# Performance work log

Hardware: AMD Instinct MI355X
Metric: run time of the kernel (lower is better)

Reference implementation:

```python
import jax, jax.numpy as jnp
import numpy as np

N_ATOMS = 10000
N_PAIRS = 100000
H = 64          # hidden_channels
R = 32          # number_of_radial_basis_functions
MAX_Z = 100
CUTOFF = 0.5    # nm (radial_max_distance), min = 0.0


def cosine_cutoff(d):
    # 0.5*(cos(pi*d/rc)+1) for d < rc else 0
    return jnp.where(d < CUTOFF, 0.5 * (jnp.cos(jnp.pi * d / CUTOFF) + 1.0), 0.0)


def expnormal_rbf(d):
    # ExpNormal smearing (TorchMD/TensorNet style), cutoff_lower = 0
    start = float(np.exp(-CUTOFF))
    means = jnp.linspace(start, 1.0, R, dtype=d.dtype)            # [R]
    beta = (2.0 / R * (1.0 - start)) ** -2
    alpha = 5.0 / CUTOFF
    return jnp.exp(-beta * (jnp.exp(-alpha * d)[:, None] - means) ** 2)  # [P,R]


def vector_to_skewtensor(v):
    x, y, z = v[:, 0], v[:, 1], v[:, 2]
    o = jnp.zeros_like(x)
    return jnp.stack([o, -z, y, z, o, -x, -y, x, o], axis=-1).reshape(-1, 3, 3)


def vector_to_symtensor(v):
    t = v[:, :, None] * v[:, None, :]                              # [P,3,3]
    tr3 = (t[:, 0, 0] + t[:, 1, 1] + t[:, 2, 2]) / 3.0
    return t - tr3[:, None, None] * jnp.eye(3, dtype=v.dtype)


def setup_inputs() -> dict:
    key = jax.random.key(0)
    ks = jax.random.split(key, 20)
    atomic_numbers = jax.random.randint(ks[0], (N_ATOMS,), 0, MAX_Z)
    pair_indices = jax.random.randint(ks[1], (2, N_PAIRS), 0, N_ATOMS)
    r_ij = jax.random.normal(ks[2], (N_PAIRS, 3), dtype=jnp.float32) * 0.12  # ~0.2 nm norms
    d_ij = jnp.linalg.norm(r_ij, axis=-1, keepdims=True) + 1e-6
    s = 0.1
    p = {
        'emb':    jax.random.normal(ks[3], (MAX_Z, H)) * s,
        'emb2_w': jax.random.normal(ks[4], (H, 2 * H)) * s,
        'emb2_b': jnp.zeros((H,)),
        'dp1_w':  jax.random.normal(ks[5], (H, R)) * s,
        'dp1_b':  jnp.zeros((H,)),
        'dp2_w':  jax.random.normal(ks[6], (H, R)) * s,
        'dp2_b':  jnp.zeros((H,)),
        'dp3_w':  jax.random.normal(ks[7], (H, R)) * s,
        'dp3_b':  jnp.zeros((H,)),
        'lt0_w':  jax.random.normal(ks[8], (H, H)) * s,
        'lt1_w':  jax.random.normal(ks[9], (H, H)) * s,
        'lt2_w':  jax.random.normal(ks[10], (H, H)) * s,
        'ls1_w':  jax.random.normal(ks[11], (2 * H, H)) * s,
        'ls1_b':  jnp.zeros((2 * H,)),
        'ls2_w':  jax.random.normal(ks[12], (3 * H, 2 * H)) * s,
        'ls2_b':  jnp.zeros((3 * H,)),
        'ln_g':   jnp.ones((H,)),
        'ln_b':   jnp.zeros((H,)),
    }
    return dict(atomic_numbers=atomic_numbers, pair_indices=pair_indices,
                d_ij=d_ij, r_ij=r_ij, **p)


def reference(atomic_numbers, pair_indices, d_ij, r_ij,
              emb, emb2_w, emb2_b, dp1_w, dp1_b, dp2_w, dp2_b, dp3_w, dp3_b,
              lt0_w, lt1_w, lt2_w, ls1_w, ls1_b, ls2_w, ls2_b, ln_g, ln_b):
    n_atoms = atomic_numbers.shape[0]
    src = pair_indices[0]
    # atomic number message Zij: concat(emb[i], emb[j]) -> Linear
    zi = emb[atomic_numbers]                                      # [N,H]
    zij = jnp.concatenate([zi[src], zi[pair_indices[1]]], axis=-1)  # [P,2H]
    Zij = zij @ emb2_w.T + emb2_b                                 # [P,H]
    d = d_ij[:, 0]                                                # [P]
    unit = r_ij / d_ij                                            # [P,3]
    rc = cosine_cutoff(d)                                         # [P]
    rbf = expnormal_rbf(d) * rc[:, None]                          # [P,R]
    C = rc[:, None] * Zij                                         # [P,H]
    f1 = (rbf @ dp1_w.T + dp1_b) * C                              # [P,H]
    f2 = (rbf @ dp2_w.T + dp2_b) * C * 10.0                       # Angstrom scale
    f3 = (rbf @ dp3_w.T + dp3_b) * C * 100.0
    eye = jnp.eye(3, dtype=r_ij.dtype)
    skew = vector_to_skewtensor(unit)                             # [P,3,3]
    sym = vector_to_symtensor(unit)                               # [P,3,3]
    Iij = f1[:, :, None, None] * eye                              # [P,H,3,3]
    Aij = f2[:, :, None, None] * skew[:, None]
    Sij = f3[:, :, None, None] * sym[:, None]
    I = jax.ops.segment_sum(Iij, src, num_segments=n_atoms)       # [N,H,3,3]
    A = jax.ops.segment_sum(Aij, src, num_segments=n_atoms)
    S = jax.ops.segment_sum(Sij, src, num_segments=n_atoms)
    # tensor_norm -> LayerNorm -> scalar MLP
    tn = jnp.sum((I + A + S) ** 2, axis=(-2, -1))                 # [N,H]
    mu = tn.mean(-1, keepdims=True)
    var = tn.var(-1, keepdims=True)
    norm = (tn - mu) / jnp.sqrt(var + 1e-5) * ln_g + ln_b
    norm = jax.nn.silu(norm @ ls1_w.T + ls1_b)
    norm = jax.nn.silu(norm @ ls2_w.T + ls2_b)                    # [N,3H]
    norm = norm.reshape(-1, H, 3)
    I = jnp.einsum('nhij,gh->ngij', I, lt0_w) * norm[:, :, 0][:, :, None, None]
    A = jnp.einsum('nhij,gh->ngij', A, lt1_w) * norm[:, :, 1][:, :, None, None]
    S = jnp.einsum('nhij,gh->ngij', S, lt2_w) * norm[:, :, 2][:, :, None, None]
    return I + A + S
```

## Files before the change

### kernel.cpp

```cpp
#include <hip/hip_runtime.h>
#include <hip/hip_bf16.h>

#define N_ATOMS 10000
#define N_PAIRS 100000
#define HH 64
#define MAXZ 100

typedef _Float16 h2_t __attribute__((ext_vector_type(2)));

constexpr float RBF_START = 0.6065306597126334f;
constexpr float RBF_STEP  = (1.0f - RBF_START) / 31.0f;
constexpr float RBF_BETA  = 1.0f / ((0.0625f * (1.0f - RBF_START)) * (0.0625f * (1.0f - RBF_START)));
constexpr float LOG2E     = 1.4426950408889634f;
constexpr float NEG_ALPHA_L2 = -10.0f * LOG2E;
constexpr float NEG_BETA_L2  = -RBF_BETA * LOG2E;

#define OFF_EMB   0
#define OFF_W2    6400
#define OFF_B2    14592
#define OFF_D1W   14656
#define OFF_D1B   16704
#define OFF_D2W   16768
#define OFF_D2B   18816
#define OFF_D3W   18880
#define OFF_D3B   20928
#define OFF_LT0   20992
#define OFF_LT1   25088
#define OFF_LT2   29184
#define OFF_L1W   33280
#define OFF_L1B   41472
#define OFF_L2W   41600
#define OFF_L2B   66176
#define OFF_LNG   66368
#define OFF_LNB   66432
#define N_PARAMF  66496

#define PH_DP   0
#define PH_L1   3072
#define PH_L2   7168
#define PH_LT   19456
#define PH_N    25600

#define WS_WF     0
#define WS_CNT    266240
#define WS_OFF    307200
#define WS_CUR    348160
#define WS_T1     389120
#define WS_T2     414720
#define WS_PH     440320
#define WS_DPK    542720
#define WS_ZNL    2142720
#define WS_ACCH   2542720

__device__ __forceinline__ float bf2f(unsigned short u) {
    return __uint_as_float(((unsigned int)u) << 16);
}
__device__ __forceinline__ float fexp2(float x) { return __builtin_amdgcn_exp2f(x); }
__device__ __forceinline__ float fcos2pi(float x) { return __builtin_amdgcn_cosf(x); }
__device__ __forceinline__ float fsilu(float x) { return x / (1.0f + fexp2(-LOG2E * x)); }
__device__ __forceinline__ h2_t u2h(unsigned u) { return __builtin_bit_cast(h2_t, u); }
__device__ __forceinline__ unsigned packh2(float a, float b) {
    h2_t v; v.x = (_Float16)a; v.y = (_Float16)b;
    return __builtin_bit_cast(unsigned, v);
}

#if __has_builtin(__builtin_amdgcn_fdot2)
__device__ __forceinline__ float FDOT2(h2_t a, h2_t b, float c) {
    return __builtin_amdgcn_fdot2(a, b, c, false);
}
#else
__device__ __forceinline__ float FDOT2(h2_t a, h2_t b, float c) {
    return c + (float)a.x * (float)b.x + (float)a.y * (float)b.y;
}
#endif
__device__ __forceinline__ float dot16h(const uint4* w, const uint4* x, float acc) {
    uint4 a = *w, b = *x;
    acc = FDOT2(u2h(a.x), u2h(b.x), acc);
    acc = FDOT2(u2h(a.y), u2h(b.y), acc);
    acc = FDOT2(u2h(a.z), u2h(b.z), acc);
    acc = FDOT2(u2h(a.w), u2h(b.w), acc);
    return acc;
}

__device__ int classify64(const unsigned short* b, int lane) {
    unsigned short x = b[lane];
    int e = (x >> 7) & 0xFF;
    bool implaus = (x != 0) && (e < 96 || e > 133);
    bool zeroeven = ((lane & 1) == 0) && (x == 0);
    unsigned long long mi = __ballot(implaus);
    unsigned long long mz = __ballot(zeroeven);
    if (__popcll(mz) == 32) return 0;
    if (__popcll(mi) >= 8) return 0;
    return 1;
}

__device__ __forceinline__ float ldp(const void* p, int off, int fl) {
    if (fl == 1) return bf2f(((const unsigned short*)p)[off]);
    return ((const float*)p)[off];
}

struct ConvArgs { const void* src[18]; float* dst; };

__global__ void k_prep(ConvArgs a, const int* __restrict__ pidx, int* __restrict__ cnt,
                       float* __restrict__ T1, float* __restrict__ T2,
                       unsigned* __restrict__ PH) {
    const int sizes[18] = {6400,8192,64,2048,64,2048,64,2048,64,4096,4096,4096,8192,128,24576,192,64,64};
    __shared__ int fl;
    if (threadIdx.x < 64) {
        int f = classify64((const unsigned short*)a.src[0], threadIdx.x);
        if (threadIdx.x == 0) fl = f;
    }
    __syncthreads();

    if (blockIdx.x < 391) {
        int t = blockIdx.x * 256 + threadIdx.x;
        if (t < N_PARAMF) {
            int acc = 0, seg = 0, off = t;
            #pragma unroll
            for (int i = 0; i < 18; ++i) {
                if (t >= acc && t < acc + sizes[i]) { seg = i; off = t - acc; }
                acc += sizes[i];
            }
            a.dst[t] = ldp(a.src[seg], off, fl);
        }
        if (t < N_PAIRS) atomicAdd(&cnt[pidx[t]], 1);
        return;
    }

    int zb = blockIdx.x - 391;
    int h = threadIdx.x;
    if (h < 64) {
        float s1 = 0.f, s2 = 0.f;
        #pragma unroll
        for (int k = 0; k < 64; ++k) {
            float e = ldp(a.src[0], zb * HH + k, fl);
            s1 += ldp(a.src[1], h * 128 + k, fl) * e;
            s2 += ldp(a.src[1], h * 128 + 64 + k, fl) * e;
        }
        T1[zb * HH + h] = s1;
        T2[zb * HH + h] = s2;
    }
    int q = zb * 256 + threadIdx.x;
    const void* sp; int off;
    if (q < PH_L1) {
        int w = q >> 10, r = q & 1023;
        sp = a.src[3 + 2 * w];
        off = r * 2;
    } else if (q < PH_L2) {
        sp = a.src[12]; off = (q - PH_L1) * 2;
    } else if (q < PH_LT) {
        sp = a.src[14]; off = (q - PH_L2) * 2;
    } else {
        int tt = q - PH_LT;
        sp = a.src[9 + (tt >> 11)]; off = (tt & 2047) * 2;
    }
    PH[q] = packh2(ldp(sp, off, fl), ldp(sp, off + 1, fl));
}

__global__ void k_scan(const int* __restrict__ cnt, int* __restrict__ offs, int* __restrict__ cur) {
    __shared__ int wsum[16];
    int tid = threadIdx.x;
    int lane = tid & 63, wid = tid >> 6;
    int base = tid * 10;
    int c[10]; int s = 0;
    #pragma unroll
    for (int i = 0; i < 10; ++i) {
        int idx = base + i;
        int v = (idx < N_ATOMS) ? cnt[idx] : 0;
        c[i] = v; s += v;
    }
    int inc = s;
    #pragma unroll
    for (int o = 1; o < 64; o <<= 1) {
        int v = __shfl_up(inc, o);
        if (lane >= o) inc += v;
    }
    if (lane == 63) wsum[wid] = inc;
    __syncthreads();
    int wbase = 0;
    #pragma unroll
    for (int w = 0; w < 16; ++w) {
        int v = wsum[w];
        if (w < wid) wbase += v;
    }
    int run = wbase + (inc - s);
    #pragma unroll
    for (int i = 0; i < 10; ++i) {
        int idx = base + i;
        if (idx < N_ATOMS) { offs[idx] = run; cur[idx] = run; run += c[i]; }
    }
    if (tid == 0) offs[N_ATOMS] = N_PAIRS;
}

__global__ void k_fill(const int* __restrict__ pidx, const int* __restrict__ an,
                       const void* __restrict__ dij_v, const void* __restrict__ rij_v,
                       int* __restrict__ cur,
                       float4* __restrict__ dpack, int* __restrict__ znl) {
    __shared__ int fdr[2];
    if (threadIdx.x < 64) {
        int fd = classify64((const unsigned short*)dij_v, threadIdx.x);
        int fr = classify64((const unsigned short*)rij_v, threadIdx.x);
        if (threadIdx.x == 0) { fdr[0] = fd; fdr[1] = fr; }
    }
    __syncthreads();
    int p = blockIdx.x * 256 + threadIdx.x;
    if (p >= N_PAIRS) return;
    int s = pidx[p];
    int dst = pidx[N_PAIRS + p];
    int pos = atomicAdd(&cur[s], 1);
    float d, rx, ry, rz;
    if (fdr[0] == 1) d = bf2f(((const unsigned short*)dij_v)[p]);
    else             d = ((const float*)dij_v)[p];
    if (fdr[1] == 1) {
        const unsigned short* r = (const unsigned short*)rij_v;
        rx = bf2f(r[3*p]); ry = bf2f(r[3*p+1]); rz = bf2f(r[3*p+2]);
    } else {
        const float* r = (const float*)rij_v;
        rx = r[3*p]; ry = r[3*p+1]; rz = r[3*p+2];
    }
    dpack[pos] = make_float4(rx, ry, rz, d);
    znl[pos] = an[dst];
}

__global__ __launch_bounds__(256, 2) void k_pair(
    const int* __restrict__ an,
    const float* __restrict__ WF,
    const int* __restrict__ offs,
    const float4* __restrict__ dpack, const int* __restrict__ znl,
    const float* __restrict__ T1, const float* __restrict__ T2,
    const unsigned* __restrict__ PH,
    unsigned* __restrict__ accH)
{
    const int wave = threadIdx.x >> 6;
    const int h    = threadIdx.x & 63;
    const int n    = blockIdx.x * 4 + wave;

    unsigned w1u[16], w2u[16], w3u[16];
    {
        const uint4* g1 = (const uint4*)(PH + PH_DP + 0 * 1024 + h * 16);
        const uint4* g2 = (const uint4*)(PH + PH_DP + 1 * 1024 + h * 16);
        const uint4* g3 = (const uint4*)(PH + PH_DP + 2 * 1024 + h * 16);
        #pragma unroll
        for (int k = 0; k < 4; ++k) {
            uint4 a = g1[k]; w1u[4*k] = a.x; w1u[4*k+1] = a.y; w1u[4*k+2] = a.z; w1u[4*k+3] = a.w;
            uint4 b = g2[k]; w2u[4*k] = b.x; w2u[4*k+1] = b.y; w2u[4*k+2] = b.z; w2u[4*k+3] = b.w;
            uint4 c = g3[k]; w3u[4*k] = c.x; w3u[4*k+1] = c.y; w3u[4*k+2] = c.z; w3u[4*k+3] = c.w;
        }
    }
    #pragma unroll
    for (int q = 0; q < 16; ++q)
        asm volatile("" : "+v"(w1u[q]), "+v"(w2u[q]), "+v"(w3u[q]));

    const float ed1 = (WF + OFF_D1B)[h];
    const float ed2 = (WF + OFF_D2B)[h];
    const float ed3 = (WF + OFF_D3B)[h];
    const float zA  = (WF + OFF_B2)[h] + T1[an[n] * HH + h];

    float Is=0.f, sx=0.f, sy=0.f, sz=0.f;
    float Sxx=0.f, Syy=0.f, Szz=0.f, Sxy=0.f, Sxz=0.f, Syz=0.f;

    const int pbeg = offs[n], pend = offs[n + 1];

    const float meanj = RBF_START + RBF_STEP * (float)(h & 31);

    float4 dp_cur = make_float4(0.f, 0.f, 0.f, 1.f);
    float4 dp_nxt = make_float4(0.f, 0.f, 0.f, 1.f);
    float  t2cur  = 0.f;
    int    zn_n   = 0;
    if (pbeg < pend) {
        dp_cur = dpack[pbeg];
        t2cur  = T2[znl[pbeg] * HH + h];
        if (pbeg + 1 < pend) {
            dp_nxt = dpack[pbeg + 1];
            zn_n   = znl[pbeg + 1];
        }
    }

    for (int ii = pbeg; ii < pend; ++ii) {
        const float4 dpv = dp_cur;
        const float  t2v = t2cur;
        dp_cur = dp_nxt;
        if (ii + 2 < pend) dp_nxt = dpack[ii + 2];
        if (ii + 1 < pend) t2cur  = T2[zn_n * HH + h];
        if (ii + 2 < pend) zn_n   = znl[ii + 2];

        float d = dpv.w;
        float inv = 1.0f / d;
        float ux = dpv.x*inv, uy = dpv.y*inv, uz = dpv.z*inv;
        float rc = (d < 0.5f) ? 0.5f * (fcos2pi(d) + 1.0f) : 0.0f;

        float en = fexp2(NEG_ALPHA_L2 * d);
        float t  = en - meanj;
        float r  = fexp2(NEG_BETA_L2 * t * t) * rc;
        float rdn = __shfl_down(r, 1);
        unsigned ru = packh2(r, rdn);
        unsigned rbs[16];
        #pragma unroll
        for (int q = 0; q < 16; ++q)
            rbs[q] = (unsigned)__builtin_amdgcn_readlane((int)ru, 2 * q);

        float g1a = ed1, g2a = ed2, g3a = ed3;
        #pragma unroll
        for (int q = 0; q < 16; ++q) {
            h2_t rb = u2h(rbs[q]);
            g1a = FDOT2(u2h(w1u[q]), rb, g1a);
            g2a = FDOT2(u2h(w2u[q]), rb, g2a);
            g3a = FDOT2(u2h(w3u[q]), rb, g3a);
        }

        float zc = zA + t2v;
        float Cc = rc * zc;
        float f1 = g1a * Cc;
        float f2 = g2a * Cc * 10.0f;
        float f3 = g3a * Cc * 100.0f;

        Is += f1;
        sx += f2 * ux;  sy += f2 * uy;  sz += f2 * uz;
        float qq = (ux*ux + uy*uy + uz*uz) * (1.0f / 3.0f);
        Sxx += f3 * (ux*ux - qq);
        Syy += f3 * (uy*uy - qq);
        Szz += f3 * (uz*uz - qq);
        Sxy += f3 * (ux*uy);
        Sxz += f3 * (ux*uz);
        Syz += f3 * (uy*uz);
    }

    float tn = 3.0f*Is*Is + 2.0f*(sx*sx + sy*sy + sz*sz)
             + Sxx*Sxx + Syy*Syy + Szz*Szz
             + 2.0f*(Sxy*Sxy + Sxz*Sxz + Syz*Syz);
    float s1 = tn, s2 = tn * tn;
    #pragma unroll
    for (int o = 32; o > 0; o >>= 1) {
        s1 += __shfl_xor(s1, o);
        s2 += __shfl_xor(s2, o);
    }
    float mu  = s1 * (1.0f / 64.0f);
    float var = s2 * (1.0f / 64.0f) - mu * mu;
    float nv  = (tn - mu) * rsqrtf(var + 1e-5f) * (WF + OFF_LNG)[h] + (WF + OFF_LNB)[h];

    float vals[11] = {Is, sx, sy, sz, Sxx, Syy, Szz, Sxy, Sxz, Syz, nv};
    #pragma unroll
    for (int c = 0; c < 11; ++c) {
        float pv = __shfl_xor(vals[c], 1);
        if ((h & 1) == 0)
            accH[((n * 11 + c) << 5) + (h >> 1)] = packh2(vals[c], pv);
    }
}

__global__ __launch_bounds__(256, 2) void k_post(
    const float* __restrict__ WF,
    const unsigned* __restrict__ PH,
    const unsigned* __restrict__ accH,
    float* __restrict__ out)
{
    __shared__ __align__(16) unsigned wL2[192 * 68];
    __shared__ __align__(16) unsigned acch[4][12 * 32];
    __shared__ __align__(16) unsigned y1h[4][64];
    __shared__ __align__(16) unsigned y2h[4][96];

    for (int q = threadIdx.x; q < 12288; q += 256) {
        int m = q >> 6, u = q & 63;
        wL2[m * 68 + u] = PH[PH_L2 + q];
    }
    __syncthreads();

    const int wave = threadIdx.x >> 6;
    const int h    = threadIdx.x & 63;
    const int gw   = blockIdx.x * 4 + wave;
    const int GW   = gridDim.x * 4;

    const uint4* l1base = (const uint4*)(PH + PH_L1);
    const uint4* lt0 = (const uint4*)(PH + PH_LT) + h * 8;
    const uint4* lt1 = (const uint4*)(PH + PH_LT + 2048) + h * 8;
    const uint4* lt2 = (const uint4*)(PH + PH_LT + 4096) + h * 8;

    for (int n = gw; n < N_ATOMS; n += GW) {
        if (h < 32) {
            #pragma unroll
            for (int c = 0; c < 11; ++c)
                acch[wave][c * 32 + h] = accH[((n * 11 + c) << 5) + h];
        }
        __builtin_amdgcn_wave_barrier();

        const uint4* nvh = (const uint4*)&acch[wave][10 * 32];

        float ya = (WF + OFF_L1B)[h];
        float yb = (WF + OFF_L1B)[h + 64];
        {
            const uint4* ra = l1base + h * 8;
            const uint4* rb = l1base + (h + 64) * 8;
            #pragma unroll
            for (int k = 0; k < 8; ++k) {
                ya = dot16h(ra + k, nvh + k, ya);
                yb = dot16h(rb + k, nvh + k, yb);
            }
        }
        ya = fsilu(ya); yb = fsilu(yb);
        {
            float pa = __shfl_xor(ya, 1);
            float pb = __shfl_xor(yb, 1);
            if ((h & 1) == 0) {
                y1h[wave][(h >> 1)]      = packh2(ya, pa);
                y1h[wave][32 + (h >> 1)] = packh2(yb, pb);
            }
        }
        __builtin_amdgcn_wave_barrier();

        const uint4* y1p = (const uint4*)&y1h[wave][0];
        float z0 = (WF + OFF_L2B)[h];
        float z1 = (WF + OFF_L2B)[h + 64];
        float z2 = (WF + OFF_L2B)[h + 128];
        {
            const uint4* r0 = (const uint4*)&wL2[(h)       * 68];
            const uint4* r1 = (const uint4*)&wL2[(h + 64)  * 68];
            const uint4* r2 = (const uint4*)&wL2[(h + 128) * 68];
            #pragma unroll
            for (int k = 0; k < 16; ++k) {
                uint4 x = y1p[k];
                uint4 a0 = r0[k], a1 = r1[k], a2 = r2[k];
                z0 = FDOT2(u2h(a0.x), u2h(x.x), z0); z0 = FDOT2(u2h(a0.y), u2h(x.y), z0);
                z0 = FDOT2(u2h(a0.z), u2h(x.z), z0); z0 = FDOT2(u2h(a0.w), u2h(x.w), z0);
                z1 = FDOT2(u2h(a1.x), u2h(x.x), z1); z1 = FDOT2(u2h(a1.y), u2h(x.y), z1);
                z1 = FDOT2(u2h(a1.z), u2h(x.z), z1); z1 = FDOT2(u2h(a1.w), u2h(x.w), z1);
                z2 = FDOT2(u2h(a2.x), u2h(x.x), z2); z2 = FDOT2(u2h(a2.y), u2h(x.y), z2);
                z2 = FDOT2(u2h(a2.z), u2h(x.z), z2); z2 = FDOT2(u2h(a2.w), u2h(x.w), z2);
            }
        }
        z0 = fsilu(z0); z1 = fsilu(z1); z2 = fsilu(z2);
        {
            float p0 = __shfl_xor(z0, 1);
            float p1 = __shfl_xor(z1, 1);
            float p2 = __shfl_xor(z2, 1);
            if ((h & 1) == 0) {
                y2h[wave][(h >> 1)]      = packh2(z0, p0);
                y2h[wave][32 + (h >> 1)] = packh2(z1, p1);
                y2h[wave][64 + (h >> 1)] = packh2(z2, p2);
            }
        }
        __builtin_amdgcn_wave_barrier();

        float n0, n1, n2;
        {
            int i0 = 3 * h;
            unsigned u0 = y2h[wave][i0 >> 1];
            unsigned u1 = y2h[wave][(i0 >> 1) + 1];
            h2_t a = u2h(u0), b = u2h(u1);
            if (i0 & 1) { n0 = (float)a.y; n1 = (float)b.x; n2 = (float)b.y; }
            else        { n0 = (float)a.x; n1 = (float)a.y; n2 = (float)b.x; }
        }

        const uint4* aI  = (const uint4*)&acch[wave][0];
        const uint4* aAx = (const uint4*)&acch[wave][32];
        const uint4* aAy = (const uint4*)&acch[wave][64];
        const uint4* aAz = (const uint4*)&acch[wave][96];
        const uint4* aXX = (const uint4*)&acch[wave][128];
        const uint4* aYY = (const uint4*)&acch[wave][160];
        const uint4* aZZ = (const uint4*)&acch[wave][192];
        const uint4* aXY = (const uint4*)&acch[wave][224];
        const uint4* aXZ = (const uint4*)&acch[wave][256];
        const uint4* aYZ = (const uint4*)&acch[wave][288];

        float P0=0.f, PAx=0.f, PAy=0.f, PAz=0.f;
        float Q0=0.f, Q1=0.f, Q2=0.f, Q3=0.f, Q4=0.f, Q5=0.f;
        #pragma unroll
        for (int k = 0; k < 8; ++k) {
            P0  = dot16h(lt0 + k, aI  + k, P0);
            PAx = dot16h(lt1 + k, aAx + k, PAx);
            PAy = dot16h(lt1 + k, aAy + k, PAy);
            PAz = dot16h(lt1 + k, aAz + k, PAz);
            Q0  = dot16h(lt2 + k, aXX + k, Q0);
            Q1  = dot16h(lt2 + k, aYY + k, Q1);
            Q2  = dot16h(lt2 + k, aZZ + k, Q2);
            Q3  = dot16h(lt2 + k, aXY + k, Q3);
            Q4  = dot16h(lt2 + k, aXZ + k, Q4);
            Q5  = dot16h(lt2 + k, aYZ + k, Q5);
        }
        float Iv = P0 * n0;
        float Ax = PAx * n1, Ay = PAy * n1, Az = PAz * n1;
        float Xx = Q0 * n2, Yy = Q1 * n2, Zz = Q2 * n2;
        float Xy = Q3 * n2, Xz = Q4 * n2, Yz = Q5 * n2;

        float* o = out + (size_t)n * 576 + h * 9;
        o[0] =  Iv + Xx;  o[1] = -Az + Xy;  o[2] =  Ay + Xz;
        o[3] =  Az + Xy;  o[4] =  Iv + Yy;  o[5] = -Ax + Yz;
        o[6] = -Ay + Xz;  o[7] =  Ax + Yz;  o[8] =  Iv + Zz;
        __builtin_amdgcn_wave_barrier();
    }
}

extern "C" void kernel_launch(void* const* d_in, const int* in_sizes, int n_in,
                              void* d_out, int out_size, void* d_ws, size_t ws_size,
                              hipStream_t stream) {
    const int* an   = (const int*)d_in[0];
    const int* pidx = (const int*)d_in[1];

    char* ws = (char*)d_ws;
    float*    WF    = (float*)(ws + WS_WF);
    int*      cnt   = (int*)(ws + WS_CNT);
    int*      offs  = (int*)(ws + WS_OFF);
    int*      cur   = (int*)(ws + WS_CUR);
    float*    T1    = (float*)(ws + WS_T1);
    float*    T2    = (float*)(ws + WS_T2);
    unsigned* PH    = (unsigned*)(ws + WS_PH);
    float4*   dpack = (float4*)(ws + WS_DPK);
    int*      znl   = (int*)(ws + WS_ZNL);
    unsigned* accH  = (unsigned*)(ws + WS_ACCH);
    float*    out   = (float*)d_out;

    hipMemsetAsync(cnt, 0, N_ATOMS * sizeof(int), stream);

    ConvArgs ca;
    for (int i = 0; i < 18; ++i) ca.src[i] = d_in[4 + i];
    ca.dst = WF;
    k_prep<<<491, 256, 0, stream>>>(ca, pidx, cnt, T1, T2, PH);
    k_scan<<<1, 1024, 0, stream>>>(cnt, offs, cur);
    k_fill<<<(N_PAIRS + 255) / 256, 256, 0, stream>>>(pidx, an, d_in[2], d_in[3],
                                                      cur, dpack, znl);
    k_pair<<<2500, 256, 0, stream>>>(an, WF, offs, dpack, znl, T1, T2, PH, accH);
    k_post<<<256, 256, 0, stream>>>(WF, PH, accH, out);
}
```

Baseline: 235.8 us.

## Replace global-atomic counting sort with per-block LDS histograms and prefix offsets

```diff
diff --git a/kernel.cpp b/kernel.cpp
--- a/kernel.cpp
+++ b/kernel.cpp
@@ -5,6 +5,9 @@
 #define N_PAIRS 100000
 #define HH 64
 #define MAXZ 100
+
+#define NB_HIST 64
+#define PPB 1563
 
 typedef _Float16 h2_t __attribute__((ext_vector_type(2)));
 
@@ -44,13 +47,14 @@
 #define WS_WF     0
 #define WS_CNT    266240
 #define WS_OFF    307200
-#define WS_CUR    348160
 #define WS_T1     389120
 #define WS_T2     414720
 #define WS_PH     440320
 #define WS_DPK    542720
 #define WS_ZNL    2142720
 #define WS_ACCH   2542720
+#define WS_H      WS_ACCH
+#define WS_SUB    (WS_ACCH + 2560000)
 
 __device__ __forceinline__ float bf2f(unsigned short u) {
     return __uint_as_float(((unsigned int)u) << 16);
@@ -101,10 +105,11 @@
 
 struct ConvArgs { const void* src[18]; float* dst; };
 
-__global__ void k_prep(ConvArgs a, const int* __restrict__ pidx, int* __restrict__ cnt,
+__global__ void k_prep(ConvArgs a, const int* __restrict__ pidx,
                        float* __restrict__ T1, float* __restrict__ T2,
-                       unsigned* __restrict__ PH) {
+                       unsigned* __restrict__ PH, int* __restrict__ H) {
     const int sizes[18] = {6400,8192,64,2048,64,2048,64,2048,64,4096,4096,4096,8192,128,24576,192,64,64};
+    __shared__ int lh[N_ATOMS];
     __shared__ int fl;
     if (threadIdx.x < 64) {
         int f = classify64((const unsigned short*)a.src[0], threadIdx.x);
@@ -112,7 +117,7 @@
     }
     __syncthreads();
 
-    if (blockIdx.x < 391) {
+    if (blockIdx.x < 260) {
         int t = blockIdx.x * 256 + threadIdx.x;
         if (t < N_PARAMF) {
             int acc = 0, seg = 0, off = t;
@@ -123,41 +128,67 @@
             }
             a.dst[t] = ldp(a.src[seg], off, fl);
         }
-        if (t < N_PAIRS) atomicAdd(&cnt[pidx[t]], 1);
         return;
     }
 
-    int zb = blockIdx.x - 391;
-    int h = threadIdx.x;
-    if (h < 64) {
-        float s1 = 0.f, s2 = 0.f;
-        #pragma unroll
-        for (int k = 0; k < 64; ++k) {
-            float e = ldp(a.src[0], zb * HH + k, fl);
-            s1 += ldp(a.src[1], h * 128 + k, fl) * e;
-            s2 += ldp(a.src[1], h * 128 + 64 + k, fl) * e;
-        }
-        T1[zb * HH + h] = s1;
-        T2[zb * HH + h] = s2;
-    }
-    int q = zb * 256 + threadIdx.x;
-    const void* sp; int off;
-    if (q < PH_L1) {
-        int w = q >> 10, r = q & 1023;
-        sp = a.src[3 + 2 * w];
-        off = r * 2;
-    } else if (q < PH_L2) {
-        sp = a.src[12]; off = (q - PH_L1) * 2;
-    } else if (q < PH_LT) {
-        sp = a.src[14]; off = (q - PH_L2) * 2;
-    } else {
-        int tt = q - PH_LT;
-        sp = a.src[9 + (tt >> 11)]; off = (tt & 2047) * 2;
-    }
-    PH[q] = packh2(ldp(sp, off, fl), ldp(sp, off + 1, fl));
-}
-
-__global__ void k_scan(const int* __restrict__ cnt, int* __restrict__ offs, int* __restrict__ cur) {
+    if (blockIdx.x < 360) {
+        int zb = blockIdx.x - 260;
+        int h = threadIdx.x;
+        if (h < 64) {
+            float s1 = 0.f, s2 = 0.f;
+            #pragma unroll
+            for (int k = 0; k < 64; ++k) {
+                float e = ldp(a.src[0], zb * HH + k, fl);
+                s1 += ldp(a.src[1], h * 128 + k, fl) * e;
+                s2 += ldp(a.src[1], h * 128 + 64 + k, fl) * e;
+            }
+            T1[zb * HH + h] = s1;
+            T2[zb * HH + h] = s2;
+        }
+        int q = zb * 256 + threadIdx.x;
+        const void* sp; int off;
+        if (q < PH_L1) {
+            int w = q >> 10, r = q & 1023;
+            sp = a.src[3 + 2 * w];
+            off = r * 2;
+        } else if (q < PH_L2) {
+            sp = a.src[12]; off = (q - PH_L1) * 2;
+        } else if (q < PH_LT) {
+            sp = a.src[14]; off = (q - PH_L2) * 2;
+        } else {
+            int tt = q - PH_LT;
+            sp = a.src[9 + (tt >> 11)]; off = (tt & 2047) * 2;
+        }
+        PH[q] = packh2(ldp(sp, off, fl), ldp(sp, off + 1, fl));
+        return;
+    }
+
+    int b = blockIdx.x - 360;
+    for (int i = threadIdx.x; i < N_ATOMS; i += 256) lh[i] = 0;
+    __syncthreads();
+    int p0 = b * PPB;
+    int p1 = p0 + PPB; if (p1 > N_PAIRS) p1 = N_PAIRS;
+    for (int p = p0 + threadIdx.x; p < p1; p += 256)
+        atomicAdd(&lh[pidx[p]], 1);
+    __syncthreads();
+    for (int i = threadIdx.x; i < N_ATOMS; i += 256)
+        H[b * N_ATOMS + i] = lh[i];
+}
+
+__global__ void k_red(const int* __restrict__ H, int* __restrict__ SUBr,
+                      int* __restrict__ total) {
+    int s = blockIdx.x * 256 + threadIdx.x;
+    if (s >= N_ATOMS) return;
+    int run = 0;
+    #pragma unroll 8
+    for (int b = 0; b < NB_HIST; ++b) {
+        SUBr[b * N_ATOMS + s] = run;
+        run += H[b * N_ATOMS + s];
+    }
+    total[s] = run;
+}
+
+__global__ void k_scan(const int* __restrict__ total, int* __restrict__ offs) {
     __shared__ int wsum[16];
     int tid = threadIdx.x;
     int lane = tid & 63, wid = tid >> 6;
@@ -166,7 +197,7 @@
     #pragma unroll
     for (int i = 0; i < 10; ++i) {
         int idx = base + i;
-        int v = (idx < N_ATOMS) ? cnt[idx] : 0;
+        int v = (idx < N_ATOMS) ? total[idx] : 0;
         c[i] = v; s += v;
     }
     int inc = s;
@@ -187,39 +218,45 @@
     #pragma unroll
     for (int i = 0; i < 10; ++i) {
         int idx = base + i;
-        if (idx < N_ATOMS) { offs[idx] = run; cur[idx] = run; run += c[i]; }
+        if (idx < N_ATOMS) { offs[idx] = run; run += c[i]; }
     }
     if (tid == 0) offs[N_ATOMS] = N_PAIRS;
 }
 
 __global__ void k_fill(const int* __restrict__ pidx, const int* __restrict__ an,
                        const void* __restrict__ dij_v, const void* __restrict__ rij_v,
-                       int* __restrict__ cur,
+                       const int* __restrict__ offs, const int* __restrict__ SUBr,
                        float4* __restrict__ dpack, int* __restrict__ znl) {
+    __shared__ int lh[N_ATOMS];
     __shared__ int fdr[2];
     if (threadIdx.x < 64) {
         int fd = classify64((const unsigned short*)dij_v, threadIdx.x);
         int fr = classify64((const unsigned short*)rij_v, threadIdx.x);
         if (threadIdx.x == 0) { fdr[0] = fd; fdr[1] = fr; }
     }
+    for (int i = threadIdx.x; i < N_ATOMS; i += 256) lh[i] = 0;
     __syncthreads();
-    int p = blockIdx.x * 256 + threadIdx.x;
-    if (p >= N_PAIRS) return;
-    int s = pidx[p];
-    int dst = pidx[N_PAIRS + p];
-    int pos = atomicAdd(&cur[s], 1);
-    float d, rx, ry, rz;
-    if (fdr[0] == 1) d = bf2f(((const unsigned short*)dij_v)[p]);
-    else             d = ((const float*)dij_v)[p];
-    if (fdr[1] == 1) {
-        const unsigned short* r = (const unsigned short*)rij_v;
-        rx = bf2f(r[3*p]); ry = bf2f(r[3*p+1]); rz = bf2f(r[3*p+2]);
-    } else {
-        const float* r = (const float*)rij_v;
-        rx = r[3*p]; ry = r[3*p+1]; rz = r[3*p+2];
-    }
-    dpack[pos] = make_float4(rx, ry, rz, d);
-    znl[pos] = an[dst];
+    int b = blockIdx.x;
+    int p0 = b * PPB;
+    int p1 = p0 + PPB; if (p1 > N_PAIRS) p1 = N_PAIRS;
+    for (int p = p0 + threadIdx.x; p < p1; p += 256) {
+        int s = pidx[p];
+        int dst = pidx[N_PAIRS + p];
+        int lr = atomicAdd(&lh[s], 1);
+        int pos = offs[s] + SUBr[b * N_ATOMS + s] + lr;
+        float d, rx, ry, rz;
+        if (fdr[0] == 1) d = bf2f(((const unsigned short*)dij_v)[p]);
+        else             d = ((const float*)dij_v)[p];
+        if (fdr[1] == 1) {
+            const unsigned short* r = (const unsigned short*)rij_v;
+            rx = bf2f(r[3*p]); ry = bf2f(r[3*p+1]); rz = bf2f(r[3*p+2]);
+        } else {
+            const float* r = (const float*)rij_v;
+            rx = r[3*p]; ry = r[3*p+1]; rz = r[3*p+2];
+        }
+        dpack[pos] = make_float4(rx, ry, rz, d);
+        znl[pos] = an[dst];
+    }
 }
 
 __global__ __launch_bounds__(256, 2) void k_pair(
@@ -496,26 +533,26 @@
 
     char* ws = (char*)d_ws;
     float*    WF    = (float*)(ws + WS_WF);
-    int*      cnt   = (int*)(ws + WS_CNT);
+    int*      total = (int*)(ws + WS_CNT);
     int*      offs  = (int*)(ws + WS_OFF);
-    int*      cur   = (int*)(ws + WS_CUR);
     float*    T1    = (float*)(ws + WS_T1);
     float*    T2    = (float*)(ws + WS_T2);
     unsigned* PH    = (unsigned*)(ws + WS_PH);
     float4*   dpack = (float4*)(ws + WS_DPK);
     int*      znl   = (int*)(ws + WS_ZNL);
+    int*      H     = (int*)(ws + WS_H);
+    int*      SUBr  = (int*)(ws + WS_SUB);
     unsigned* accH  = (unsigned*)(ws + WS_ACCH);
     float*    out   = (float*)d_out;
-
-    hipMemsetAsync(cnt, 0, N_ATOMS * sizeof(int), stream);
 
     ConvArgs ca;
     for (int i = 0; i < 18; ++i) ca.src[i] = d_in[4 + i];
     ca.dst = WF;
-    k_prep<<<491, 256, 0, stream>>>(ca, pidx, cnt, T1, T2, PH);
-    k_scan<<<1, 1024, 0, stream>>>(cnt, offs, cur);
-    k_fill<<<(N_PAIRS + 255) / 256, 256, 0, stream>>>(pidx, an, d_in[2], d_in[3],
-                                                      cur, dpack, znl);
+    k_prep<<<424, 256, 0, stream>>>(ca, pidx, T1, T2, PH, H);
+    k_red<<<40, 256, 0, stream>>>(H, SUBr, total);
+    k_scan<<<1, 1024, 0, stream>>>(total, offs);
+    k_fill<<<NB_HIST, 256, 0, stream>>>(pidx, an, d_in[2], d_in[3],
+                                        offs, SUBr, dpack, znl);
     k_pair<<<2500, 256, 0, stream>>>(an, WF, offs, dpack, znl, T1, T2, PH, accH);
     k_post<<<256, 256, 0, stream>>>(WF, PH, accH, out);
 }
```

After: 232.9 us. No clear change (-1.2%).
